# Kernel tuning notes

Measured on AMD Instinct MI355X. Metric: run time of the kernel, lower is better.

## Reference

```python
import jax, jax.numpy as jnp
import numpy as np

TOKENS, DIM, N_EXPERTS, TOPK = 8192, 4096, 256, 8

def setup_inputs() -> dict:
    key = jax.random.key(0)
    k1, k2 = jax.random.split(key)
    x = jax.random.normal(k1, (TOKENS, DIM), dtype=jnp.float32)
    weight = jax.random.normal(k2, (N_EXPERTS, DIM), dtype=jnp.float32) * (DIM ** -0.5)
    return {"x": x, "weight": weight}

def reference(x, weight):
    # logits: [tokens, n_experts]
    logits = jnp.einsum('td,ed->te', x, weight)
    scores = jax.nn.sigmoid(logits)
    topv, indices = jax.lax.top_k(scores, TOPK)          # [tokens, topk]
    gates = topv / jnp.sum(topv, axis=-1, keepdims=True)
    return gates, indices
```

## Files before the change

### kernel.cpp

```cpp
#include <hip/hip_runtime.h>
#include <hip/hip_bf16.h>
#include <hip/hip_fp16.h>
#include <math.h>

#define TOKENS   8192
#define DIM      4096
#define NEXP     256
#define TOPK     8
#define CAND     12

#define MT4      64
#define BK3      64
#define KG       (DIM / 32)

typedef _Float16 f16x8 __attribute__((ext_vector_type(8)));
typedef float    f32x4 __attribute__((ext_vector_type(4)));

typedef const __attribute__((address_space(1))) unsigned int* gas_ptr;
typedef       __attribute__((address_space(3))) unsigned int* las_ptr;

__global__ __launch_bounds__(256)
void convert_w(const float* __restrict__ w, _Float16* __restrict__ whs) {
    const int g = blockIdx.x * 256 + threadIdx.x;
    const int tile = g >> 6, c = g & 63;
    const int q = c >> 4, r = c & 15;
    const int ng = tile / KG, kg = tile % KG;
    const int n = ng * 16 + r, k = kg * 32 + q * 8;
    const float4 a = *(const float4*)(w + (size_t)n * DIM + k);
    const float4 b = *(const float4*)(w + (size_t)n * DIM + k + 4);
    f16x8 h;
    h[0] = (_Float16)a.x; h[1] = (_Float16)a.y;
    h[2] = (_Float16)a.z; h[3] = (_Float16)a.w;
    h[4] = (_Float16)b.x; h[5] = (_Float16)b.y;
    h[6] = (_Float16)b.z; h[7] = (_Float16)b.w;
    *(f16x8*)(whs + (size_t)g * 8) = h;
}

__global__ __launch_bounds__(256, 3)
void gemm_v4(const float* __restrict__ x, const _Float16* __restrict__ whs,
             float* __restrict__ logits, int kspan) {
    __shared__ _Float16 As[8 * 512];
    __shared__ _Float16 Bs[32 * 512];

    const int t = threadIdx.x, w = t >> 6, lane = t & 63;
    const int m0 = blockIdx.x * MT4;
    const int kb = blockIdx.y * kspan;
    float* lp    = logits + (size_t)blockIdx.y * TOKENS * NEXP;

    const int am  = t >> 2;
    const int ack = (t & 3) * 2;
    const int amg = am >> 4, amr = am & 15;
    const int aoff0 = ((amg * 2 + (ack >> 2)) * 64 + (ack & 3) * 16 + amr) * 8;
    const int ack1  = ack + 1;
    const int aoff1 = ((amg * 2 + (ack1 >> 2)) * 64 + (ack1 & 3) * 16 + amr) * 8;

    f32x4 acc[4][4];
    #pragma unroll
    for (int i = 0; i < 4; ++i)
        #pragma unroll
        for (int j = 0; j < 4; ++j) acc[i][j] = (f32x4){0.f, 0.f, 0.f, 0.f};

    const float* xrow = x + (size_t)(m0 + am) * DIM + ack * 8;
    f32x4 xr0 = __builtin_nontemporal_load((const f32x4*)(xrow + kb));
    f32x4 xr1 = __builtin_nontemporal_load((const f32x4*)(xrow + kb + 4));
    f32x4 xr2 = __builtin_nontemporal_load((const f32x4*)(xrow + kb + 8));
    f32x4 xr3 = __builtin_nontemporal_load((const f32x4*)(xrow + kb + 12));

    for (int k0 = kb; k0 < kb + kspan; k0 += BK3) {
        #pragma unroll
        for (int c = 0; c < 8; ++c) {
            const int ti  = w * 8 + c;
            const int ng  = ti >> 1, kgl = ti & 1;
            const _Float16* gp = whs + ((size_t)(ng * KG + (k0 >> 5) + kgl)) * 512
                                     + lane * 8;
            __builtin_amdgcn_global_load_lds((gas_ptr)gp, (las_ptr)&Bs[ti * 512],
                                             16, 0, 0);
        }
        {
            f16x8 h0, h1;
            h0[0] = (_Float16)xr0.x; h0[1] = (_Float16)xr0.y;
            h0[2] = (_Float16)xr0.z; h0[3] = (_Float16)xr0.w;
            h0[4] = (_Float16)xr1.x; h0[5] = (_Float16)xr1.y;
            h0[6] = (_Float16)xr1.z; h0[7] = (_Float16)xr1.w;
            h1[0] = (_Float16)xr2.x; h1[1] = (_Float16)xr2.y;
            h1[2] = (_Float16)xr2.z; h1[3] = (_Float16)xr2.w;
            h1[4] = (_Float16)xr3.x; h1[5] = (_Float16)xr3.y;
            h1[6] = (_Float16)xr3.z; h1[7] = (_Float16)xr3.w;
            *(f16x8*)&As[aoff0] = h0;
            *(f16x8*)&As[aoff1] = h1;
        }
        __syncthreads();

        if (k0 + BK3 < kb + kspan) {
            xr0 = __builtin_nontemporal_load((const f32x4*)(xrow + k0 + BK3));
            xr1 = __builtin_nontemporal_load((const f32x4*)(xrow + k0 + BK3 + 4));
            xr2 = __builtin_nontemporal_load((const f32x4*)(xrow + k0 + BK3 + 8));
            xr3 = __builtin_nontemporal_load((const f32x4*)(xrow + k0 + BK3 + 12));
        }

        #pragma unroll
        for (int kk = 0; kk < 2; ++kk) {
            f16x8 af[4], bf[4];
            #pragma unroll
            for (int mt = 0; mt < 4; ++mt)
                af[mt] = *(const f16x8*)&As[((mt * 2 + kk) * 64 + lane) * 8];
            #pragma unroll
            for (int nt = 0; nt < 4; ++nt)
                bf[nt] = *(const f16x8*)&Bs[(((w * 4 + nt) * 2 + kk) * 64 + lane) * 8];
            #pragma unroll
            for (int mt = 0; mt < 4; ++mt)
                #pragma unroll
                for (int nt = 0; nt < 4; ++nt)
                    acc[mt][nt] = __builtin_amdgcn_mfma_f32_16x16x32_f16(
                        af[mt], bf[nt], acc[mt][nt], 0, 0, 0);
        }
        __syncthreads();
    }

    #pragma unroll
    for (int mt = 0; mt < 4; ++mt) {
        #pragma unroll
        for (int nt = 0; nt < 4; ++nt) {
            #pragma unroll
            for (int r = 0; r < 4; ++r) {
                const int m = m0 + mt * 16 + (lane >> 4) * 4 + r;
                const int n = (w * 4 + nt) * 16 + (lane & 15);
                lp[(size_t)m * NEXP + n] = acc[mt][nt][r];
            }
        }
    }
}

__global__ __launch_bounds__(256)
void topk_cand(const float* __restrict__ logits, int* __restrict__ cand,
               int nsplit) {
    const int lane  = threadIdx.x & 63;
    const int token = blockIdx.x * 4 + (threadIdx.x >> 6);
    const float* lp = logits + (size_t)token * NEXP;

    float s[4];
    #pragma unroll
    for (int j = 0; j < 4; ++j) s[j] = 0.f;
    for (int p = 0; p < nsplit; ++p) {
        const float* pp = lp + (size_t)p * TOKENS * NEXP;
        #pragma unroll
        for (int j = 0; j < 4; ++j)
            s[j] += __builtin_nontemporal_load(pp + j * 64 + lane);
    }

    int mye = 0;
    #pragma unroll
    for (int r = 0; r < CAND; ++r) {
        float bv = s[0];
        int   be = lane;
        #pragma unroll
        for (int j = 1; j < 4; ++j) {
            if (s[j] > bv) { bv = s[j]; be = j * 64 + lane; }
        }
        #pragma unroll
        for (int off = 32; off > 0; off >>= 1) {
            const float ov = __shfl_xor(bv, off, 64);
            const int   oe = __shfl_xor(be, off, 64);
            if (ov > bv || (ov == bv && oe < be)) { bv = ov; be = oe; }
        }
        if (lane == r) mye = be;
        if ((be & 63) == lane) s[be >> 6] = -1e30f;
    }

    if (lane < CAND) cand[token * CAND + lane] = mye;
}

__global__ __launch_bounds__(256)
void rescore(const float* __restrict__ x, const float* __restrict__ w,
             const int* __restrict__ cand, float* __restrict__ out) {
    __shared__ float  xs[DIM];
    __shared__ double stot[CAND];
    __shared__ int    sce[CAND];

    const int t = threadIdx.x, wave = t >> 6, lane = t & 63;
    const int token = blockIdx.x;

    const float* xrow = x + (size_t)token * DIM;
    #pragma unroll
    for (int r = 0; r < 4; ++r) {
        const float* gp = xrow + r * 1024 + wave * 256 + lane * 4;
        __builtin_amdgcn_global_load_lds((gas_ptr)gp,
                                         (las_ptr)&xs[r * 1024 + wave * 256],
                                         16, 0, 0);
    }

    int ce[3];
    const f32x4* wp[3];
    #pragma unroll
    for (int j = 0; j < 3; ++j) {
        ce[j] = __builtin_amdgcn_readfirstlane(cand[token * CAND + wave * 3 + j]);
        wp[j] = (const f32x4*)(w + (size_t)ce[j] * DIM);
    }

    double acc[3];
    #pragma unroll
    for (int j = 0; j < 3; ++j) acc[j] = 0.0;

    f32x4 wb[2][3];
    #pragma unroll
    for (int j = 0; j < 3; ++j) wb[0][j] = wp[j][lane];

    __syncthreads();

    #pragma unroll
    for (int i = 0; i < 16; ++i) {
        const int cur = i & 1, nxt = cur ^ 1;
        if (i < 15) {
            const int o = lane + (i + 1) * 64;
            #pragma unroll
            for (int j = 0; j < 3; ++j) wb[nxt][j] = wp[j][o];
        }
        const f32x4 xv = *(const f32x4*)&xs[(lane + i * 64) * 4];
        const double dx = (double)xv.x, dy = (double)xv.y;
        const double dz = (double)xv.z, dw = (double)xv.w;
        #pragma unroll
        for (int j = 0; j < 3; ++j) {
            const f32x4 wv = wb[cur][j];
            acc[j] = fma(dw, (double)wv.w,
                     fma(dz, (double)wv.z,
                     fma(dy, (double)wv.y,
                     fma(dx, (double)wv.x, acc[j]))));
        }
    }

    #pragma unroll
    for (int off = 32; off > 0; off >>= 1) {
        #pragma unroll
        for (int j = 0; j < 3; ++j)
            acc[j] += __shfl_xor(acc[j], off, 64);
    }

    if (lane == 0) {
        #pragma unroll
        for (int j = 0; j < 3; ++j) {
            stot[wave * 3 + j] = acc[j];
            sce[wave * 3 + j]  = ce[j];
        }
    }
    __syncthreads();

    if (wave == 0) {
        double tt[CAND];
        int    ee[CAND];
        #pragma unroll
        for (int c = 0; c < CAND; ++c) { tt[c] = stot[c]; ee[c] = sce[c]; }

        int rank[CAND];
        #pragma unroll
        for (int c = 0; c < CAND; ++c) {
            int r = 0;
            #pragma unroll
            for (int j = 0; j < CAND; ++j) {
                if (j == c) continue;
                if (tt[j] > tt[c] || (tt[j] == tt[c] && ee[j] < ee[c])) ++r;
            }
            rank[c] = r;
        }

        float sig[CAND];
        float sum = 0.f;
        #pragma unroll
        for (int c = 0; c < CAND; ++c) {
            sig[c] = 1.0f / (1.0f + expf(-(float)tt[c]));
            if (rank[c] < TOPK) sum += sig[c];
        }

        if (lane < TOPK) {
            float g = 0.f; int ei = 0;
            #pragma unroll
            for (int c = 0; c < CAND; ++c)
                if (rank[c] == lane) { g = sig[c]; ei = ee[c]; }
            out[(size_t)token * TOPK + lane] = g / sum;
            out[(size_t)TOKENS * TOPK + (size_t)token * TOPK + lane] = (float)ei;
        }
    }
}

extern "C" void kernel_launch(void* const* d_in, const int* in_sizes, int n_in,
                              void* d_out, int out_size, void* d_ws, size_t ws_size,
                              hipStream_t stream) {
    const float* x = (const float*)d_in[0];
    const float* w = (const float*)d_in[1];
    float* out     = (float*)d_out;

    const size_t plane = (size_t)TOKENS * NEXP * sizeof(float);
    const size_t fixed = (size_t)TOKENS * CAND * sizeof(int)
                       + (size_t)NEXP * DIM * sizeof(_Float16);
    int S = 4;
    if (ws_size < 4 * plane + fixed) S = (ws_size >= 2 * plane + fixed) ? 2 : 1;

    float*     logits = (float*)d_ws;
    int*       candp  = (int*)((char*)d_ws + (size_t)S * plane);
    _Float16*  whs    = (_Float16*)((char*)candp + (size_t)TOKENS * CAND * sizeof(int));

    convert_w<<<512, 256, 0, stream>>>(w, whs);
    dim3 ggrid(TOKENS / MT4, S);
    gemm_v4<<<ggrid, 256, 0, stream>>>(x, whs, logits, DIM / S);
    topk_cand<<<TOKENS / 4, 256, 0, stream>>>(logits, candp, S);
    rescore<<<TOKENS, 256, 0, stream>>>(x, w, candp, out);
}
```

Baseline: 334.9 us.

## Split fp64 candidate rescoring along K into partial blocks plus finalize kernel

The per-token rescoring kernel is split into two kernels. The first launches 8 blocks per token, each computing fp64 partial dot products over a 512-wide K slice. The second sums the partials and does rank, sigmoid and normalisation with one wave per token. The goal is more parallelism and more loads in flight for the latency-bound rescoring pass, at the cost of an extra launch and a round trip of the partial results through memory. The partials reuse the logits region of the workspace, which is safe only because the logits are dead once top-k candidates are chosen.

```diff
diff --git a/kernel.cpp b/kernel.cpp
--- a/kernel.cpp
+++ b/kernel.cpp
@@ -12,6 +12,9 @@
 #define MT4      64
 #define BK3      64
 #define KG       (DIM / 32)
+
+#define KSL      8
+#define KSW      (DIM / KSL)
 
 typedef _Float16 f16x8 __attribute__((ext_vector_type(8)));
 typedef float    f32x4 __attribute__((ext_vector_type(4)));
@@ -171,22 +174,18 @@
 }
 
 __global__ __launch_bounds__(256)
-void rescore(const float* __restrict__ x, const float* __restrict__ w,
-             const int* __restrict__ cand, float* __restrict__ out) {
-    __shared__ float  xs[DIM];
-    __shared__ double stot[CAND];
-    __shared__ int    sce[CAND];
-
-    const int t = threadIdx.x, wave = t >> 6, lane = t & 63;
-    const int token = blockIdx.x;
-
-    const float* xrow = x + (size_t)token * DIM;
-    #pragma unroll
-    for (int r = 0; r < 4; ++r) {
-        const float* gp = xrow + r * 1024 + wave * 256 + lane * 4;
-        __builtin_amdgcn_global_load_lds((gas_ptr)gp,
-                                         (las_ptr)&xs[r * 1024 + wave * 256],
-                                         16, 0, 0);
+void rescore_part(const float* __restrict__ x, const float* __restrict__ w,
+                  const int* __restrict__ cand, double* __restrict__ part) {
+    __shared__ float xs[KSW];
+
+    const int s     = blockIdx.x;
+    const int token = blockIdx.y;
+    const int wave  = threadIdx.x >> 6, lane = threadIdx.x & 63;
+
+    if (wave < 2) {
+        const float* gp = x + (size_t)token * DIM + s * KSW + wave * 256 + lane * 4;
+        __builtin_amdgcn_global_load_lds((gas_ptr)gp, (las_ptr)&xs[wave * 256],
+                                         16, 0, 2 );
     }
 
     int ce[3];
@@ -194,38 +193,38 @@
     #pragma unroll
     for (int j = 0; j < 3; ++j) {
         ce[j] = __builtin_amdgcn_readfirstlane(cand[token * CAND + wave * 3 + j]);
-        wp[j] = (const f32x4*)(w + (size_t)ce[j] * DIM);
-    }
+        wp[j] = (const f32x4*)(w + (size_t)ce[j] * DIM + s * KSW);
+    }
+
+    f32x4 wv0[3], wv1[3];
+    #pragma unroll
+    for (int j = 0; j < 3; ++j) {
+        wv0[j] = wp[j][lane];
+        wv1[j] = wp[j][64 + lane];
+    }
+
+    __syncthreads();
+
+    const f32x4 x0 = *(const f32x4*)&xs[lane * 4];
+    const f32x4 x1 = *(const f32x4*)&xs[256 + lane * 4];
+    const double a0 = (double)x0.x, a1 = (double)x0.y;
+    const double a2 = (double)x0.z, a3 = (double)x0.w;
+    const double b0 = (double)x1.x, b1 = (double)x1.y;
+    const double b2 = (double)x1.z, b3 = (double)x1.w;
 
     double acc[3];
     #pragma unroll
-    for (int j = 0; j < 3; ++j) acc[j] = 0.0;
-
-    f32x4 wb[2][3];
-    #pragma unroll
-    for (int j = 0; j < 3; ++j) wb[0][j] = wp[j][lane];
-
-    __syncthreads();
-
-    #pragma unroll
-    for (int i = 0; i < 16; ++i) {
-        const int cur = i & 1, nxt = cur ^ 1;
-        if (i < 15) {
-            const int o = lane + (i + 1) * 64;
-            #pragma unroll
-            for (int j = 0; j < 3; ++j) wb[nxt][j] = wp[j][o];
-        }
-        const f32x4 xv = *(const f32x4*)&xs[(lane + i * 64) * 4];
-        const double dx = (double)xv.x, dy = (double)xv.y;
-        const double dz = (double)xv.z, dw = (double)xv.w;
-        #pragma unroll
-        for (int j = 0; j < 3; ++j) {
-            const f32x4 wv = wb[cur][j];
-            acc[j] = fma(dw, (double)wv.w,
-                     fma(dz, (double)wv.z,
-                     fma(dy, (double)wv.y,
-                     fma(dx, (double)wv.x, acc[j]))));
-        }
+    for (int j = 0; j < 3; ++j) {
+        const f32x4 u = wv0[j], v = wv1[j];
+        double t0;
+        t0 = fma(a3, (double)u.w,
+             fma(a2, (double)u.z,
+             fma(a1, (double)u.y,
+             fma(a0, (double)u.x, 0.0))));
+        acc[j] = fma(b3, (double)v.w,
+                 fma(b2, (double)v.z,
+                 fma(b1, (double)v.y,
+                 fma(b0, (double)v.x, t0))));
     }
 
     #pragma unroll
@@ -237,47 +236,63 @@
 
     if (lane == 0) {
         #pragma unroll
-        for (int j = 0; j < 3; ++j) {
-            stot[wave * 3 + j] = acc[j];
-            sce[wave * 3 + j]  = ce[j];
-        }
-    }
-    __syncthreads();
-
-    if (wave == 0) {
-        double tt[CAND];
-        int    ee[CAND];
-        #pragma unroll
-        for (int c = 0; c < CAND; ++c) { tt[c] = stot[c]; ee[c] = sce[c]; }
-
-        int rank[CAND];
-        #pragma unroll
-        for (int c = 0; c < CAND; ++c) {
-            int r = 0;
-            #pragma unroll
-            for (int j = 0; j < CAND; ++j) {
-                if (j == c) continue;
-                if (tt[j] > tt[c] || (tt[j] == tt[c] && ee[j] < ee[c])) ++r;
-            }
-            rank[c] = r;
-        }
-
-        float sig[CAND];
-        float sum = 0.f;
-        #pragma unroll
-        for (int c = 0; c < CAND; ++c) {
-            sig[c] = 1.0f / (1.0f + expf(-(float)tt[c]));
-            if (rank[c] < TOPK) sum += sig[c];
-        }
-
-        if (lane < TOPK) {
-            float g = 0.f; int ei = 0;
-            #pragma unroll
-            for (int c = 0; c < CAND; ++c)
-                if (rank[c] == lane) { g = sig[c]; ei = ee[c]; }
-            out[(size_t)token * TOPK + lane] = g / sum;
-            out[(size_t)TOKENS * TOPK + (size_t)token * TOPK + lane] = (float)ei;
-        }
+        for (int j = 0; j < 3; ++j)
+            part[((size_t)token * CAND + wave * 3 + j) * KSL + s] = acc[j];
+    }
+}
+
+__global__ __launch_bounds__(256)
+void rescore_fin(const double* __restrict__ part, const int* __restrict__ cand,
+                 float* __restrict__ out) {
+    const int wave = threadIdx.x >> 6, lane = threadIdx.x & 63;
+    const int token = blockIdx.x * 4 + wave;
+
+    double tot = -1e300;
+    int    ee  = 0x7fffffff;
+    if (lane < CAND) {
+        const double* pp = part + ((size_t)token * CAND + lane) * KSL;
+        double t = 0.0;
+        #pragma unroll
+        for (int s = 0; s < KSL; ++s) t += pp[s];
+        tot = t;
+        ee  = cand[token * CAND + lane];
+    }
+
+    double tt[CAND];
+    int    ei[CAND];
+    #pragma unroll
+    for (int j = 0; j < CAND; ++j) {
+        tt[j] = __shfl(tot, j, 64);
+        ei[j] = __shfl(ee,  j, 64);
+    }
+
+    int rank[CAND];
+    #pragma unroll
+    for (int c = 0; c < CAND; ++c) {
+        int r = 0;
+        #pragma unroll
+        for (int j = 0; j < CAND; ++j) {
+            if (j == c) continue;
+            if (tt[j] > tt[c] || (tt[j] == tt[c] && ei[j] < ei[c])) ++r;
+        }
+        rank[c] = r;
+    }
+
+    float sig[CAND];
+    float sum = 0.f;
+    #pragma unroll
+    for (int c = 0; c < CAND; ++c) {
+        sig[c] = 1.0f / (1.0f + expf(-(float)tt[c]));
+        if (rank[c] < TOPK) sum += sig[c];
+    }
+
+    if (lane < TOPK) {
+        float g = 0.f; int eo = 0;
+        #pragma unroll
+        for (int c = 0; c < CAND; ++c)
+            if (rank[c] == lane) { g = sig[c]; eo = ei[c]; }
+        out[(size_t)token * TOPK + lane] = g / sum;
+        out[(size_t)TOKENS * TOPK + (size_t)token * TOPK + lane] = (float)eo;
     }
 }
 
@@ -297,10 +312,13 @@
     float*     logits = (float*)d_ws;
     int*       candp  = (int*)((char*)d_ws + (size_t)S * plane);
     _Float16*  whs    = (_Float16*)((char*)candp + (size_t)TOKENS * CAND * sizeof(int));
+    double*    part   = (double*)d_ws;
 
     convert_w<<<512, 256, 0, stream>>>(w, whs);
     dim3 ggrid(TOKENS / MT4, S);
     gemm_v4<<<ggrid, 256, 0, stream>>>(x, whs, logits, DIM / S);
     topk_cand<<<TOKENS / 4, 256, 0, stream>>>(logits, candp, S);
-    rescore<<<TOKENS, 256, 0, stream>>>(x, w, candp, out);
-}
+    dim3 rgrid(KSL, TOKENS);
+    rescore_part<<<rgrid, 256, 0, stream>>>(x, w, candp, part);
+    rescore_fin<<<TOKENS / 4, 256, 0, stream>>>(part, candp, out);
+}
```

After: 371.1 us. 1.11x slower.
